# Kernel optimization log

Measured on AMD Instinct MI355X. Metric: run time of the kernel, lower is better.

The kernel has to match this reference:

```python
import jax, jax.numpy as jnp
import numpy as np

IN_DIM = 1024
OUT_DIM = 1024
NUM_EXPERTS = 8
TOP_K = 2
B = 8192


def setup_inputs() -> dict:
    key = jax.random.key(0)
    ks = jax.random.split(key, 8)
    s_in = 1.0 / np.sqrt(IN_DIM)
    s_out = 1.0 / np.sqrt(OUT_DIM)
    return {
        "x": jax.random.normal(ks[0], (B, IN_DIM), dtype=jnp.float32),
        # router Linear(in_dim, num_experts)
        "rw": jax.random.uniform(ks[1], (IN_DIM, NUM_EXPERTS), jnp.float32, -s_in, s_in),
        "rb": jax.random.uniform(ks[2], (NUM_EXPERTS,), jnp.float32, -s_in, s_in),
        # expert MLPs stacked along expert axis
        "w1": jax.random.uniform(ks[3], (NUM_EXPERTS, IN_DIM, OUT_DIM), jnp.float32, -s_in, s_in),
        "b1": jax.random.uniform(ks[4], (NUM_EXPERTS, OUT_DIM), jnp.float32, -s_in, s_in),
        "w2": jax.random.uniform(ks[5], (NUM_EXPERTS, OUT_DIM, OUT_DIM), jnp.float32, -s_out, s_out),
        "b2": jax.random.uniform(ks[6], (NUM_EXPERTS, OUT_DIM), jnp.float32, -s_out, s_out),
    }


def reference(x, rw, rb, w1, b1, w2, b2):
    # ---- TopkRouter ----
    logits = x @ rw + rb                                  # [B, E]
    topk_vals, topk_idx = jax.lax.top_k(logits, TOP_K)    # [B, K]
    neg_inf = jnp.full_like(logits, -jnp.inf)
    rows = jnp.arange(logits.shape[0])[:, None]
    sparse_logits = neg_inf.at[rows, topk_idx].set(topk_vals)
    gating = jax.nn.softmax(sparse_logits, axis=-1)       # zeros outside top-k

    # ---- experts: dense compute, gating weights are exactly 0 for
    # non-selected experts so the weighted combine matches the masked
    # dispatch of the original module. ----
    h = jax.nn.relu(jnp.einsum('bi,eio->beo', x, w1) + b1[None])   # [B, E, out]
    y = jnp.einsum('beh,eho->beo', h, w2) + b2[None]               # [B, E, out]
    fused = jnp.einsum('beo,be->bo', y, gating)                    # [B, out]
    return fused, gating
```

## Files before the change

kernel.cpp:

```cpp
#include <hip/hip_runtime.h>
#include <hip/hip_bf16.h>
#include <cstdint>
#include <cstddef>

#define IN_DIM 1024
#define OUT_DIM 1024
#define NE 8
#define NTOK 8192

typedef __bf16 bf16x8 __attribute__((ext_vector_type(8)));
typedef float f32x4 __attribute__((ext_vector_type(4)));
typedef unsigned short ushort8v __attribute__((ext_vector_type(8)));

__device__ __forceinline__ unsigned short f2bf(float f) {
    unsigned u = __float_as_uint(f);
    unsigned r = 0x7fffu + ((u >> 16) & 1u);
    return (unsigned short)((u + r) >> 16);
}

__device__ __forceinline__ void bf2x(unsigned u, float& lo, float& hi) {
    lo = __uint_as_float(u << 16);
    hi = __uint_as_float(u & 0xffff0000u);
}

__device__ __forceinline__ void async16(void* lds, const void* g) {
    __builtin_amdgcn_global_load_lds(
        (const __attribute__((address_space(1))) unsigned int*)g,
        (__attribute__((address_space(3))) unsigned int*)lds,
        16, 0, 0);
}

__global__ __launch_bounds__(256) void convert_transpose_kernel(
    const float* __restrict__ w1, const float* __restrict__ w2,
    unsigned short* __restrict__ w1T, unsigned short* __restrict__ w2T) {
    __shared__ float tile[64][68];
    int z = blockIdx.z;
    const float* src = (z < 8) ? (w1 + (size_t)z * IN_DIM * OUT_DIM)
                               : (w2 + (size_t)(z - 8) * OUT_DIM * OUT_DIM);
    unsigned short* dst = (z < 8) ? (w1T + (size_t)z * IN_DIM * OUT_DIM)
                                  : (w2T + (size_t)(z - 8) * OUT_DIM * OUT_DIM);
    int kt = blockIdx.x * 64, nt = blockIdx.y * 64;
    int t = threadIdx.x;
    int r = t >> 2, cq = (t & 3) * 16;
#pragma unroll
    for (int q = 0; q < 4; ++q) {
        float4 v = *(const float4*)(src + (size_t)(kt + r) * 1024 + nt + cq + q * 4);
        tile[r][cq + q * 4 + 0] = v.x;
        tile[r][cq + q * 4 + 1] = v.y;
        tile[r][cq + q * 4 + 2] = v.z;
        tile[r][cq + q * 4 + 3] = v.w;
    }
    __syncthreads();
    int n = t >> 2, kq = (t & 3) * 16;
#pragma unroll
    for (int q = 0; q < 2; ++q) {
        ushort8v o;
#pragma unroll
        for (int i = 0; i < 8; ++i) o[i] = f2bf(tile[kq + q * 8 + i][n]);
        *(ushort8v*)(dst + (size_t)(nt + n) * 1024 + kt + kq + q * 8) = o;
    }
}

__global__ __launch_bounds__(256) void router_kernel(
    const float* __restrict__ x, const float* __restrict__ rw,
    const float* __restrict__ rb,
    unsigned short* __restrict__ xb,
    float* __restrict__ gating, int* __restrict__ enc,
    float2* __restrict__ gw, int* __restrict__ cnt) {
    __shared__ float srw[NE * IN_DIM];
    int t = threadIdx.x;
    if (blockIdx.x == 0 && t < NE) cnt[t] = 0;
#pragma unroll
    for (int i = 0; i < 4; ++i) {
        int k = t + i * 256;
        float4 a = *(const float4*)(rw + (size_t)k * NE);
        float4 b = *(const float4*)(rw + (size_t)k * NE + 4);
        srw[0 * IN_DIM + k] = a.x; srw[1 * IN_DIM + k] = a.y;
        srw[2 * IN_DIM + k] = a.z; srw[3 * IN_DIM + k] = a.w;
        srw[4 * IN_DIM + k] = b.x; srw[5 * IN_DIM + k] = b.y;
        srw[6 * IN_DIM + k] = b.z; srw[7 * IN_DIM + k] = b.w;
    }
    __syncthreads();
    int wave = t >> 6, lane = t & 63;
    int tok = blockIdx.x * 4 + wave;
    const float* xrow = x + (size_t)tok * IN_DIM;
    unsigned short* xbrow = xb + (size_t)tok * IN_DIM;
    float acc[NE] = {0, 0, 0, 0, 0, 0, 0, 0};
#pragma unroll
    for (int i = 0; i < 4; ++i) {
        int k = i * 256 + lane * 4;
        float4 xv = *(const float4*)(xrow + k);
        ushort4 o;
        o.x = f2bf(xv.x); o.y = f2bf(xv.y); o.z = f2bf(xv.z); o.w = f2bf(xv.w);
        *(ushort4*)(xbrow + k) = o;
#pragma unroll
        for (int e = 0; e < NE; ++e) {
            float4 wv = *(const float4*)(srw + e * IN_DIM + k);
            acc[e] = fmaf(xv.x, wv.x, fmaf(xv.y, wv.y, fmaf(xv.z, wv.z, fmaf(xv.w, wv.w, acc[e]))));
        }
    }
#pragma unroll
    for (int e = 0; e < NE; ++e) {
#pragma unroll
        for (int off = 32; off > 0; off >>= 1) acc[e] += __shfl_xor(acc[e], off);
        acc[e] += rb[e];
    }
    int e0 = 0; float v0 = acc[0];
#pragma unroll
    for (int e = 1; e < NE; ++e) if (acc[e] > v0) { v0 = acc[e]; e0 = e; }
    int e1 = -1; float v1 = -3.4e38f;
#pragma unroll
    for (int e = 0; e < NE; ++e) if (e != e0 && acc[e] > v1) { v1 = acc[e]; e1 = e; }
    float tg = __expf(v1 - v0);
    float inv = 1.0f / (1.0f + tg);
    float g0 = inv, g1 = tg * inv;
    if (lane < NE) gating[(size_t)tok * NE + lane] = (lane == e0) ? g0 : ((lane == e1) ? g1 : 0.0f);
    if (lane == 0) {
        enc[tok] = e0 | (e1 << 8);
        gw[tok] = make_float2(g0, g1);
    }
}

__global__ __launch_bounds__(256) void bucket_kernel(
    const int* __restrict__ enc,
    int* __restrict__ bidx, int* __restrict__ slots, int* __restrict__ cnt) {
    int tok = blockIdx.x * 256 + threadIdx.x;
    int lane = threadIdx.x & 63;
    int v = enc[tok];
    int e0 = v & 0xff, e1 = (v >> 8) & 0xff;
    unsigned long long below = (1ull << lane) - 1ull;
    int p0 = 0, p1 = 0;
#pragma unroll
    for (int e = 0; e < NE; ++e) {
        unsigned long long m0 = __ballot(e0 == e);
        unsigned long long m1 = __ballot(e1 == e);
        int c0 = __popcll(m0), c1 = __popcll(m1);
        int base = 0;
        if (lane == 0 && (c0 + c1)) base = atomicAdd(&cnt[e], c0 + c1);
        base = __shfl(base, 0);
        if (e0 == e) p0 = base + __popcll(m0 & below);
        if (e1 == e) p1 = base + c0 + __popcll(m1 & below);
    }
    bidx[e0 * NTOK + p0] = tok;
    bidx[e1 * NTOK + p1] = tok;
    slots[2 * tok + 0] = (e0 << 13) | p0;
    slots[2 * tok + 1] = (e1 << 13) | p1;
}

__device__ __forceinline__ int prefix_cnt(const int* __restrict__ cnt, int e) {
    int s = 0;
    for (int i = 0; i < NE; ++i) s += (i < e) ? cnt[i] : 0;
    return s;
}


__global__ __launch_bounds__(256) void gemm1_kernel(
    const unsigned short* __restrict__ xb, const unsigned short* __restrict__ w1T,
    const float* __restrict__ b1, const int* __restrict__ bidx,
    const int* __restrict__ cnt,
    unsigned short* __restrict__ H) {
    int b = blockIdx.x;
    int e = b & 7;
    int t2 = b >> 3;
    int nt = t2 & 7;
    int mt = t2 >> 3;
    int n_e = cnt[e];
    if (mt * 128 >= n_e) return;
    __shared__ __attribute__((aligned(16))) unsigned short As[2][64 * 64];
    __shared__ __attribute__((aligned(16))) unsigned short Bs[2][64 * 64];
    int t = threadIdx.x, wave = t >> 6, lane = t & 63;
    const int* be = bidx + e * NTOK;
    const unsigned short* agp[2]; const unsigned short* bgp[2];
    int ldsoff[2];
#pragma unroll
    for (int is = 0; is < 2; ++is) {
        int c = is * 256 + t;
        int line = c >> 3;
        int chunkg = (c & 7) ^ (line & 7);
        int sub = chunkg >> 2;
        int growl = 2 * line + sub;
        int growlB = (line >> 5) * 64 + (line & 7) * 8 + sub * 4 + ((line >> 3) & 3);
        int gcol = (chunkg & 3) * 8;
        int gra = mt * 128 + growl;
        int grac = gra < n_e ? gra : n_e - 1;
        agp[is] = xb + (size_t)be[grac] * IN_DIM + gcol;
        bgp[is] = w1T + ((size_t)e * OUT_DIM + nt * 128 + growlB) * IN_DIM + gcol;
        ldsoff[is] = (is * 256 + wave * 64) * 8;
    }
    int wm = wave & 1, wn = wave >> 1;
    int quad = lane >> 4, l15 = lane & 15;
    int lhalf = l15 >> 1;
    int slot = (((l15 & 1) * 4 + quad) ^ lhalf) * 8;
    f32x4 zero4 = {0.f, 0.f, 0.f, 0.f};
    f32x4 acc[4][4];
#pragma unroll
    for (int i = 0; i < 4; ++i)
#pragma unroll
        for (int j = 0; j < 4; ++j) acc[i][j] = zero4;

#pragma unroll
    for (int is = 0; is < 2; ++is) {
        async16(&As[0][ldsoff[is]], agp[is]);
        async16(&Bs[0][ldsoff[is]], bgp[is]);
    }
    for (int it = 0; it < 32; ++it) {
        __syncthreads();
        int buf = it & 1;
        if (it + 1 < 32) {
            int ktn = (it + 1) * 32;
#pragma unroll
            for (int is = 0; is < 2; ++is) {
                async16(&As[buf ^ 1][ldsoff[is]], agp[is] + ktn);
                async16(&Bs[buf ^ 1][ldsoff[is]], bgp[is] + ktn);
            }
        }
        const unsigned short* Ab = As[buf];
        const unsigned short* Bb = Bs[buf];
        bf16x8 av[4], bv[4];
#pragma unroll
        for (int i = 0; i < 4; ++i) {
            int lineA = wm * 32 + i * 8 + lhalf;
            av[i] = *(const bf16x8*)(Ab + lineA * 64 + slot);
        }
#pragma unroll
        for (int j = 0; j < 4; ++j) {
            int lineB = wn * 32 + j * 8 + lhalf;
            bv[j] = *(const bf16x8*)(Bb + lineB * 64 + slot);
        }
#pragma unroll
        for (int i = 0; i < 4; ++i)
#pragma unroll
            for (int j = 0; j < 4; ++j)
                acc[i][j] = __builtin_amdgcn_mfma_f32_16x16x32_bf16(av[i], bv[j], acc[i][j], 0, 0, 0);
    }
    int hbase = prefix_cnt(cnt, e);
    const float* b1e = b1 + (size_t)e * OUT_DIM;
    int n0 = nt * 128 + wn * 64 + l15 * 4;
    float4 bias = *(const float4*)(b1e + n0);
#pragma unroll
    for (int i = 0; i < 4; ++i) {
        int m0 = mt * 128 + wm * 64 + i * 16 + quad * 4;
#pragma unroll
        for (int r = 0; r < 4; ++r) {
            int gm = m0 + r;
            if (gm < n_e) {
                float h0 = acc[i][0][r] + bias.x; h0 = h0 > 0.f ? h0 : 0.f;
                float h1 = acc[i][1][r] + bias.y; h1 = h1 > 0.f ? h1 : 0.f;
                float h2 = acc[i][2][r] + bias.z; h2 = h2 > 0.f ? h2 : 0.f;
                float h3 = acc[i][3][r] + bias.w; h3 = h3 > 0.f ? h3 : 0.f;
                ushort4 o;
                o.x = f2bf(h0); o.y = f2bf(h1); o.z = f2bf(h2); o.w = f2bf(h3);
                *(ushort4*)(H + (size_t)(hbase + gm) * OUT_DIM + n0) = o;
            }
        }
    }
}

__global__ __launch_bounds__(256) void gemm2_kernel(
    const unsigned short* __restrict__ H, const unsigned short* __restrict__ w2T,
    const int* __restrict__ cnt,
    unsigned short* __restrict__ Y) {
    int b = blockIdx.x;
    int e = b & 7;
    int t2 = b >> 3;
    int nt = t2 & 7;
    int mt = t2 >> 3;
    int n_e = cnt[e];
    if (mt * 128 >= n_e) return;
    __shared__ __attribute__((aligned(16))) unsigned short As[2][64 * 64];
    __shared__ __attribute__((aligned(16))) unsigned short Bs[2][64 * 64];
    int t = threadIdx.x, wave = t >> 6, lane = t & 63;
    int hbase = prefix_cnt(cnt, e);
    const unsigned short* agp[2]; const unsigned short* bgp[2];
    int ldsoff[2];
#pragma unroll
    for (int is = 0; is < 2; ++is) {
        int c = is * 256 + t;
        int line = c >> 3;
        int chunkg = (c & 7) ^ (line & 7);
        int sub = chunkg >> 2;
        int growl = 2 * line + sub;
        int growlB = (line >> 5) * 64 + (line & 7) * 8 + sub * 4 + ((line >> 3) & 3);
        int gcol = (chunkg & 3) * 8;
        int gra = mt * 128 + growl;
        int grac = gra < n_e ? gra : n_e - 1;
        agp[is] = H + (size_t)(hbase + grac) * OUT_DIM + gcol;
        bgp[is] = w2T + ((size_t)e * OUT_DIM + nt * 128 + growlB) * OUT_DIM + gcol;
        ldsoff[is] = (is * 256 + wave * 64) * 8;
    }
    int wm = wave & 1, wn = wave >> 1;
    int quad = lane >> 4, l15 = lane & 15;
    int lhalf = l15 >> 1;
    int slot = (((l15 & 1) * 4 + quad) ^ lhalf) * 8;
    f32x4 zero4 = {0.f, 0.f, 0.f, 0.f};
    f32x4 acc[4][4];
#pragma unroll
    for (int i = 0; i < 4; ++i)
#pragma unroll
        for (int j = 0; j < 4; ++j) acc[i][j] = zero4;

#pragma unroll
    for (int is = 0; is < 2; ++is) {
        async16(&As[0][ldsoff[is]], agp[is]);
        async16(&Bs[0][ldsoff[is]], bgp[is]);
    }
    for (int it = 0; it < 32; ++it) {
        __syncthreads();
        int buf = it & 1;
        if (it + 1 < 32) {
            int ktn = (it + 1) * 32;
#pragma unroll
            for (int is = 0; is < 2; ++is) {
                async16(&As[buf ^ 1][ldsoff[is]], agp[is] + ktn);
                async16(&Bs[buf ^ 1][ldsoff[is]], bgp[is] + ktn);
            }
        }
        const unsigned short* Ab = As[buf];
        const unsigned short* Bb = Bs[buf];
        bf16x8 av[4], bv[4];
#pragma unroll
        for (int i = 0; i < 4; ++i) {
            int lineA = wm * 32 + i * 8 + lhalf;
            av[i] = *(const bf16x8*)(Ab + lineA * 64 + slot);
        }
#pragma unroll
        for (int j = 0; j < 4; ++j) {
            int lineB = wn * 32 + j * 8 + lhalf;
            bv[j] = *(const bf16x8*)(Bb + lineB * 64 + slot);
        }
#pragma unroll
        for (int i = 0; i < 4; ++i)
#pragma unroll
            for (int j = 0; j < 4; ++j)
                acc[i][j] = __builtin_amdgcn_mfma_f32_16x16x32_bf16(av[i], bv[j], acc[i][j], 0, 0, 0);
    }
    int n0 = nt * 128 + wn * 64 + l15 * 4;
#pragma unroll
    for (int i = 0; i < 4; ++i) {
        int m0 = mt * 128 + wm * 64 + i * 16 + quad * 4;
#pragma unroll
        for (int r = 0; r < 4; ++r) {
            int gm = m0 + r;
            if (gm < n_e) {
                ushort4 o;
                o.x = f2bf(acc[i][0][r]); o.y = f2bf(acc[i][1][r]);
                o.z = f2bf(acc[i][2][r]); o.w = f2bf(acc[i][3][r]);
                *(ushort4*)(Y + (size_t)(hbase + gm) * OUT_DIM + n0) = o;
            }
        }
    }
}

__global__ __launch_bounds__(256) void combine_kernel(
    const unsigned short* __restrict__ Y, const float* __restrict__ b2,
    const float2* __restrict__ gw, const int* __restrict__ slots,
    const int* __restrict__ cnt, float* __restrict__ out) {
    int t = threadIdx.x, wave = t >> 6, lane = t & 63;
    int tok = blockIdx.x * 4 + wave;
    int pre[NE];
    {
        int s = 0;
#pragma unroll
        for (int i = 0; i < NE; ++i) { pre[i] = s; s += cnt[i]; }
    }
    int s0 = slots[2 * tok], s1 = slots[2 * tok + 1];
    int e0 = s0 >> 13, e1 = s1 >> 13;
    int r0 = pre[e0] + (s0 & 8191);
    int r1 = pre[e1] + (s1 & 8191);
    float2 g = gw[tok];
    const unsigned short* y0 = Y + (size_t)r0 * OUT_DIM;
    const unsigned short* y1 = Y + (size_t)r1 * OUT_DIM;
    const float* c0 = b2 + (size_t)e0 * OUT_DIM;
    const float* c1 = b2 + (size_t)e1 * OUT_DIM;
    float* orow = out + (size_t)tok * OUT_DIM;
#pragma unroll
    for (int i = 0; i < 2; ++i) {
        int c = i * 512 + lane * 8;
        uint4 ua = *(const uint4*)(y0 + c);
        uint4 ub = *(const uint4*)(y1 + c);
        float a[8], b[8];
        bf2x(ua.x, a[0], a[1]); bf2x(ua.y, a[2], a[3]);
        bf2x(ua.z, a[4], a[5]); bf2x(ua.w, a[6], a[7]);
        bf2x(ub.x, b[0], b[1]); bf2x(ub.y, b[2], b[3]);
        bf2x(ub.z, b[4], b[5]); bf2x(ub.w, b[6], b[7]);
        float4 p0 = *(const float4*)(c0 + c);
        float4 p1 = *(const float4*)(c0 + c + 4);
        float4 q0 = *(const float4*)(c1 + c);
        float4 q1 = *(const float4*)(c1 + c + 4);
        float o[8];
        o[0] = g.x * (a[0] + p0.x) + g.y * (b[0] + q0.x);
        o[1] = g.x * (a[1] + p0.y) + g.y * (b[1] + q0.y);
        o[2] = g.x * (a[2] + p0.z) + g.y * (b[2] + q0.z);
        o[3] = g.x * (a[3] + p0.w) + g.y * (b[3] + q0.w);
        o[4] = g.x * (a[4] + p1.x) + g.y * (b[4] + q1.x);
        o[5] = g.x * (a[5] + p1.y) + g.y * (b[5] + q1.y);
        o[6] = g.x * (a[6] + p1.z) + g.y * (b[6] + q1.z);
        o[7] = g.x * (a[7] + p1.w) + g.y * (b[7] + q1.w);
        *(float4*)(orow + c) = make_float4(o[0], o[1], o[2], o[3]);
        *(float4*)(orow + c + 4) = make_float4(o[4], o[5], o[6], o[7]);
    }
}

extern "C" void kernel_launch(void* const* d_in, const int* in_sizes, int n_in,
                              void* d_out, int out_size, void* d_ws, size_t ws_size,
                              hipStream_t stream) {
    const float* x  = (const float*)d_in[0];
    const float* rw = (const float*)d_in[1];
    const float* rb = (const float*)d_in[2];
    const float* w1 = (const float*)d_in[3];
    const float* b1 = (const float*)d_in[4];
    const float* w2 = (const float*)d_in[5];
    const float* b2 = (const float*)d_in[6];
    float* out = (float*)d_out;
    float* gating = out + (size_t)NTOK * OUT_DIM;

    char* ws = (char*)d_ws;
    unsigned short* xb  = (unsigned short*)(ws + 0);
    unsigned short* Y   = (unsigned short*)(ws + 0);
    unsigned short* w1T = (unsigned short*)(ws + 16777216);
    unsigned short* w2T = (unsigned short*)(ws + 33554432);
    unsigned short* H   = (unsigned short*)(ws + 50331648);
    int*   bidx  = (int*)(ws + 83886080);
    int*   slots = (int*)(ws + 84148224);
    int*   cnt   = (int*)(ws + 84213760);
    int*    enc  = (int*)(ws + 84213888);
    float2* gw   = (float2*)(ws + 84246656);

    convert_transpose_kernel<<<dim3(16, 16, 16), 256, 0, stream>>>(w1, w2, w1T, w2T);
    router_kernel<<<NTOK / 4, 256, 0, stream>>>(x, rw, rb, xb, gating, enc, gw, cnt);
    bucket_kernel<<<NTOK / 256, 256, 0, stream>>>(enc, bidx, slots, cnt);
    gemm1_kernel<<<8 * 8 * 64, 256, 0, stream>>>(xb, w1T, b1, bidx, cnt, H);
    gemm2_kernel<<<8 * 8 * 64, 256, 0, stream>>>(H, w2T, cnt, Y);
    combine_kernel<<<NTOK / 4, 256, 0, stream>>>(Y, b2, gw, slots, cnt, out);
    (void)in_sizes; (void)n_in; (void)out_size; (void)ws_size;
}
```

Baseline: 298.4 us.

## Deepen GEMM async LDS pipeline to four stages with counted vmcnt waits

Both expert GEMM kernels move from a double-buffered LDS pipeline to a four-buffer ring that keeps three K-tiles of global-to-LDS loads in flight. The full __syncthreads is replaced by an explicit s_waitcnt vmcnt(8) plus s_barrier so a wave waits only for the oldest tile, and the last two tiles are drained in an epilogue. The goal is to hide global memory latency better; in exchange LDS use doubles to 64 KB per block, which can lower occupancy, and correctness depends on the hand-counted vmcnt values.

```diff
diff --git a/kernel.cpp b/kernel.cpp
--- a/kernel.cpp
+++ b/kernel.cpp
@@ -153,6 +153,24 @@
     return s;
 }
 
+__device__ __forceinline__ void kstep(const unsigned short* Ab,
+                                      const unsigned short* Bb,
+                                      f32x4 (&acc)[4][4], int wm, int wn,
+                                      int lhalf, int slot) {
+    bf16x8 av[4], bv[4];
+#pragma unroll
+    for (int i = 0; i < 4; ++i)
+        av[i] = *(const bf16x8*)(Ab + (wm * 32 + i * 8 + lhalf) * 64 + slot);
+#pragma unroll
+    for (int j = 0; j < 4; ++j)
+        bv[j] = *(const bf16x8*)(Bb + (wn * 32 + j * 8 + lhalf) * 64 + slot);
+#pragma unroll
+    for (int i = 0; i < 4; ++i)
+#pragma unroll
+        for (int j = 0; j < 4; ++j)
+            acc[i][j] = __builtin_amdgcn_mfma_f32_16x16x32_bf16(av[i], bv[j], acc[i][j], 0, 0, 0);
+}
+
 
 __global__ __launch_bounds__(256) void gemm1_kernel(
     const unsigned short* __restrict__ xb, const unsigned short* __restrict__ w1T,
@@ -166,8 +184,8 @@
     int mt = t2 >> 3;
     int n_e = cnt[e];
     if (mt * 128 >= n_e) return;
-    __shared__ __attribute__((aligned(16))) unsigned short As[2][64 * 64];
-    __shared__ __attribute__((aligned(16))) unsigned short Bs[2][64 * 64];
+    __shared__ __attribute__((aligned(16))) unsigned short As[4][64 * 64];
+    __shared__ __attribute__((aligned(16))) unsigned short Bs[4][64 * 64];
     int t = threadIdx.x, wave = t >> 6, lane = t & 63;
     const int* be = bidx + e * NTOK;
     const unsigned short* agp[2]; const unsigned short* bgp[2];
@@ -199,40 +217,29 @@
         for (int j = 0; j < 4; ++j) acc[i][j] = zero4;
 
 #pragma unroll
-    for (int is = 0; is < 2; ++is) {
-        async16(&As[0][ldsoff[is]], agp[is]);
-        async16(&Bs[0][ldsoff[is]], bgp[is]);
-    }
-    for (int it = 0; it < 32; ++it) {
-        __syncthreads();
-        int buf = it & 1;
-        if (it + 1 < 32) {
-            int ktn = (it + 1) * 32;
+    for (int pt = 0; pt < 3; ++pt)
+#pragma unroll
+        for (int is = 0; is < 2; ++is) {
+            async16(&As[pt][ldsoff[is]], agp[is] + pt * 32);
+            async16(&Bs[pt][ldsoff[is]], bgp[is] + pt * 32);
+        }
+    for (int it = 0; it < 30; ++it) {
+        asm volatile("s_waitcnt vmcnt(8)\n\ts_barrier" ::: "memory");
+        if (it < 29) {
+            int nb = (it + 3) & 3, ktn = (it + 3) * 32;
 #pragma unroll
             for (int is = 0; is < 2; ++is) {
-                async16(&As[buf ^ 1][ldsoff[is]], agp[is] + ktn);
-                async16(&Bs[buf ^ 1][ldsoff[is]], bgp[is] + ktn);
+                async16(&As[nb][ldsoff[is]], agp[is] + ktn);
+                async16(&Bs[nb][ldsoff[is]], bgp[is] + ktn);
             }
         }
-        const unsigned short* Ab = As[buf];
-        const unsigned short* Bb = Bs[buf];
-        bf16x8 av[4], bv[4];
-#pragma unroll
-        for (int i = 0; i < 4; ++i) {
-            int lineA = wm * 32 + i * 8 + lhalf;
-            av[i] = *(const bf16x8*)(Ab + lineA * 64 + slot);
-        }
-#pragma unroll
-        for (int j = 0; j < 4; ++j) {
-            int lineB = wn * 32 + j * 8 + lhalf;
-            bv[j] = *(const bf16x8*)(Bb + lineB * 64 + slot);
-        }
-#pragma unroll
-        for (int i = 0; i < 4; ++i)
-#pragma unroll
-            for (int j = 0; j < 4; ++j)
-                acc[i][j] = __builtin_amdgcn_mfma_f32_16x16x32_bf16(av[i], bv[j], acc[i][j], 0, 0, 0);
-    }
+        kstep(As[it & 3], Bs[it & 3], acc, wm, wn, lhalf, slot);
+    }
+    asm volatile("s_waitcnt vmcnt(4)\n\ts_barrier" ::: "memory");
+    kstep(As[2], Bs[2], acc, wm, wn, lhalf, slot);
+    asm volatile("s_waitcnt vmcnt(0)\n\ts_barrier" ::: "memory");
+    kstep(As[3], Bs[3], acc, wm, wn, lhalf, slot);
+
     int hbase = prefix_cnt(cnt, e);
     const float* b1e = b1 + (size_t)e * OUT_DIM;
     int n0 = nt * 128 + wn * 64 + l15 * 4;
@@ -267,8 +274,8 @@
     int mt = t2 >> 3;
     int n_e = cnt[e];
     if (mt * 128 >= n_e) return;
-    __shared__ __attribute__((aligned(16))) unsigned short As[2][64 * 64];
-    __shared__ __attribute__((aligned(16))) unsigned short Bs[2][64 * 64];
+    __shared__ __attribute__((aligned(16))) unsigned short As[4][64 * 64];
+    __shared__ __attribute__((aligned(16))) unsigned short Bs[4][64 * 64];
     int t = threadIdx.x, wave = t >> 6, lane = t & 63;
     int hbase = prefix_cnt(cnt, e);
     const unsigned short* agp[2]; const unsigned short* bgp[2];
@@ -300,40 +307,29 @@
         for (int j = 0; j < 4; ++j) acc[i][j] = zero4;
 
 #pragma unroll
-    for (int is = 0; is < 2; ++is) {
-        async16(&As[0][ldsoff[is]], agp[is]);
-        async16(&Bs[0][ldsoff[is]], bgp[is]);
-    }
-    for (int it = 0; it < 32; ++it) {
-        __syncthreads();
-        int buf = it & 1;
-        if (it + 1 < 32) {
-            int ktn = (it + 1) * 32;
+    for (int pt = 0; pt < 3; ++pt)
+#pragma unroll
+        for (int is = 0; is < 2; ++is) {
+            async16(&As[pt][ldsoff[is]], agp[is] + pt * 32);
+            async16(&Bs[pt][ldsoff[is]], bgp[is] + pt * 32);
+        }
+    for (int it = 0; it < 30; ++it) {
+        asm volatile("s_waitcnt vmcnt(8)\n\ts_barrier" ::: "memory");
+        if (it < 29) {
+            int nb = (it + 3) & 3, ktn = (it + 3) * 32;
 #pragma unroll
             for (int is = 0; is < 2; ++is) {
-                async16(&As[buf ^ 1][ldsoff[is]], agp[is] + ktn);
-                async16(&Bs[buf ^ 1][ldsoff[is]], bgp[is] + ktn);
+                async16(&As[nb][ldsoff[is]], agp[is] + ktn);
+                async16(&Bs[nb][ldsoff[is]], bgp[is] + ktn);
             }
         }
-        const unsigned short* Ab = As[buf];
-        const unsigned short* Bb = Bs[buf];
-        bf16x8 av[4], bv[4];
-#pragma unroll
-        for (int i = 0; i < 4; ++i) {
-            int lineA = wm * 32 + i * 8 + lhalf;
-            av[i] = *(const bf16x8*)(Ab + lineA * 64 + slot);
-        }
-#pragma unroll
-        for (int j = 0; j < 4; ++j) {
-            int lineB = wn * 32 + j * 8 + lhalf;
-            bv[j] = *(const bf16x8*)(Bb + lineB * 64 + slot);
-        }
-#pragma unroll
-        for (int i = 0; i < 4; ++i)
-#pragma unroll
-            for (int j = 0; j < 4; ++j)
-                acc[i][j] = __builtin_amdgcn_mfma_f32_16x16x32_bf16(av[i], bv[j], acc[i][j], 0, 0, 0);
-    }
+        kstep(As[it & 3], Bs[it & 3], acc, wm, wn, lhalf, slot);
+    }
+    asm volatile("s_waitcnt vmcnt(4)\n\ts_barrier" ::: "memory");
+    kstep(As[2], Bs[2], acc, wm, wn, lhalf, slot);
+    asm volatile("s_waitcnt vmcnt(0)\n\ts_barrier" ::: "memory");
+    kstep(As[3], Bs[3], acc, wm, wn, lhalf, slot);
+
     int n0 = nt * 128 + wn * 64 + l15 * 4;
 #pragma unroll
     for (int i = 0; i < 4; ++i) {
```

Measured after the change: 328.5 us. +10.1%, slower.
